# Performance work log

Measured on AMD Instinct MI355X. Metric: run time of the kernel, lower is better.

## Reference

```python
import jax, jax.numpy as jnp
import numpy as np

D_MODEL = 1024
N_HEADS = 16
D_K = D_MODEL // N_HEADS


def setup_inputs() -> dict:
    key = jax.random.key(0)
    ks = jax.random.split(key, 10)
    B, S = 4, 2048
    std = 1.0 / np.sqrt(D_MODEL)
    inp = {
        "x": jax.random.normal(ks[0], (B, S, D_MODEL), dtype=jnp.float32),
        "attention_mask": jnp.ones((B, S), dtype=jnp.int32),
        "W_q": jax.random.normal(ks[1], (D_MODEL, D_MODEL), dtype=jnp.float32) * std,
        "b_q": jnp.zeros((D_MODEL,), dtype=jnp.float32),
        "W_k": jax.random.normal(ks[2], (D_MODEL, D_MODEL), dtype=jnp.float32) * std,
        "b_k": jnp.zeros((D_MODEL,), dtype=jnp.float32),
        "W_v": jax.random.normal(ks[3], (D_MODEL, D_MODEL), dtype=jnp.float32) * std,
        "b_v": jnp.zeros((D_MODEL,), dtype=jnp.float32),
        "W_o": jax.random.normal(ks[4], (D_MODEL, D_MODEL), dtype=jnp.float32) * std,
        "b_o": jnp.zeros((D_MODEL,), dtype=jnp.float32),
    }
    return inp


def reference(x, attention_mask, W_q, b_q, W_k, b_k, W_v, b_v, W_o, b_o):
    B, S, _ = x.shape
    # projections -> [B, H, S, d_k]
    def proj(W, b):
        return (x @ W.T + b).reshape(B, S, N_HEADS, D_K).transpose(0, 2, 1, 3)
    q = proj(W_q, b_q)
    k = proj(W_k, b_k)
    v = proj(W_v, b_v)
    scores = jnp.einsum("bhqd,bhkd->bhqk", q, k) / jnp.sqrt(jnp.float32(D_K))
    mask = attention_mask[:, None, None, :] == 0  # [B,1,1,S]
    scores = jnp.where(mask, -jnp.inf, scores)
    probs = jax.nn.softmax(scores, axis=-1)  # dropout p=0 (eval)
    out = jnp.einsum("bhqk,bhkd->bhqd", probs, v)
    out = out.transpose(0, 2, 1, 3).reshape(B, S, D_MODEL)
    return out @ W_o.T + b_o
```

## Files before the change

kernel.cpp:

```cpp
#include <hip/hip_runtime.h>
#include <hip/hip_bf16.h>


#define SEQ   2048
#define DM    1024
#define NH    16
#define DK    64
#define MTOT  8192

typedef unsigned short u16;
typedef __attribute__((ext_vector_type(8))) short bf16x8;
typedef __attribute__((ext_vector_type(4))) float f32x4;

typedef union { unsigned u[4]; bf16x8 v; } FragU;

#define MFMA(a, b, c) __builtin_amdgcn_mfma_f32_16x16x32_bf16((a), (b), (c), 0, 0, 0)

#if __has_builtin(__builtin_amdgcn_exp2f)
#define EXP2(x) __builtin_amdgcn_exp2f(x)
#else
#define EXP2(x) __expf((x) * 0.69314718056f)
#endif

__device__ __forceinline__ u16 f2bf(float v) {
    unsigned int x = __float_as_uint(v);
    x += 0x7fffu + ((x >> 16) & 1u);
    return (u16)(x >> 16);
}
__device__ __forceinline__ float bf2f(u16 u) {
    return __uint_as_float(((unsigned int)u) << 16);
}
__device__ __forceinline__ unsigned pk2bf(float a, float b) {
    __hip_bfloat162 t = __float22bfloat162_rn(make_float2(a, b));
    unsigned r;
    __builtin_memcpy(&r, &t, 4);
    return r;
}

__device__ __forceinline__ void gl_lds16(const void* g, void* l) {
    __builtin_amdgcn_global_load_lds((__attribute__((address_space(1))) void*)g,
                                     (__attribute__((address_space(3))) void*)l,
                                     16, 0, 0);
}

__global__ __launch_bounds__(256) void split_f32(const float* __restrict__ src,
                                                 u16* __restrict__ dh,
                                                 u16* __restrict__ dl, int n4) {
    int i = blockIdx.x * 256 + threadIdx.x;
    if (i >= n4) return;
    float4 v = ((const float4*)src)[i];
    const float* f = (const float*)&v;
    ushort4 hh, ll;
    u16* hp = (u16*)&hh;
    u16* lp = (u16*)&ll;
#pragma unroll
    for (int j = 0; j < 4; ++j) {
        u16 h = f2bf(f[j]);
        hp[j] = h;
        lp[j] = f2bf(f[j] - bf2f(h));
    }
    ((ushort4*)dh)[i] = hh;
    ((ushort4*)dl)[i] = ll;
}

template <int MODE>
__global__ __launch_bounds__(256, 2) void gemm_split(
    const u16* __restrict__ Ah, const u16* __restrict__ Al,
    const u16* __restrict__ Bh, const u16* __restrict__ Bl,
    const float* __restrict__ bias,
    float* __restrict__ outF, u16* __restrict__ outH, u16* __restrict__ outL) {
    __shared__ u16 sm[4][128 * 64];

    const int tid = threadIdx.x;
    const int w = tid >> 6, lane = tid & 63;
    const int n0 = blockIdx.x * 128, m0 = blockIdx.y * 128;
    const int wr = w >> 1, wc = w & 1;
    const int rowoff = lane >> 3;
    const int cswz = ((lane & 7) ^ rowoff) << 3;

    const u16* src = (w == 0) ? Ah : (w == 1) ? Al : (w == 2) ? Bh : Bl;
    const int row0 = (w < 2) ? m0 : n0;
    const u16* sbase = src + (size_t)(row0 + rowoff) * 1024 + cswz;

    f32x4 acc[4][4];
#pragma unroll
    for (int a = 0; a < 4; ++a)
#pragma unroll
        for (int b = 0; b < 4; ++b) acc[a][b] = (f32x4)0.f;

    for (int k0 = 0; k0 < 1024; k0 += 64) {
#pragma unroll
        for (int i = 0; i < 16; ++i)
            gl_lds16(sbase + (size_t)(8 * i) * 1024 + k0, &sm[w][i * 512]);
        __syncthreads();
#pragma unroll
        for (int kk = 0; kk < 2; ++kk) {
            bf16x8 ah[4], al[4], bh[4], bl[4];
#pragma unroll
            for (int t = 0; t < 4; ++t) {
                const int Ra = wr * 64 + t * 16 + (lane & 15);
                const int oa = Ra * 128 + ((((kk << 2) + (lane >> 4)) ^ (Ra & 7)) << 4);
                ah[t] = *(const bf16x8*)((const char*)&sm[0][0] + oa);
                al[t] = *(const bf16x8*)((const char*)&sm[1][0] + oa);
                const int Rb = wc * 64 + t * 16 + (lane & 15);
                const int ob = Rb * 128 + ((((kk << 2) + (lane >> 4)) ^ (Rb & 7)) << 4);
                bh[t] = *(const bf16x8*)((const char*)&sm[2][0] + ob);
                bl[t] = *(const bf16x8*)((const char*)&sm[3][0] + ob);
            }
#pragma unroll
            for (int mt = 0; mt < 4; ++mt)
#pragma unroll
                for (int nt = 0; nt < 4; ++nt) {
                    acc[mt][nt] = MFMA(ah[mt], bh[nt], acc[mt][nt]);
                    acc[mt][nt] = MFMA(ah[mt], bl[nt], acc[mt][nt]);
                    acc[mt][nt] = MFMA(al[mt], bh[nt], acc[mt][nt]);
                }
        }
        __syncthreads();
    }

#pragma unroll
    for (int mt = 0; mt < 4; ++mt) {
#pragma unroll
        for (int nt = 0; nt < 4; ++nt) {
            const int n = n0 + wc * 64 + nt * 16 + (lane & 15);
            const float bv = bias[n];
#pragma unroll
            for (int j = 0; j < 4; ++j) {
                const int m = m0 + wr * 64 + mt * 16 + (lane >> 4) * 4 + j;
                const float v = acc[mt][nt][j] + bv;
                if (MODE == 0) {
                    outF[(size_t)m * 1024 + n] = v;
                } else {
                    const u16 h16 = f2bf(v);
                    const u16 l16 = f2bf(v - bf2f(h16));
                    const int b = m >> 11, s = m & 2047, hh = n >> 6, dk = n & 63;
                    size_t idx;
                    if (MODE == 1) idx = (((size_t)(b * 16 + hh)) * 2048 + s) * 64 + dk;
                    else           idx = (((size_t)(b * 16 + hh)) * 64 + dk) * 2048 + s;
                    outH[idx] = h16;
                    outL[idx] = l16;
                }
            }
        }
    }
}

__global__ __launch_bounds__(256, 2) void flash_mfma4(
    const u16* __restrict__ Qh, const u16* __restrict__ Ql,
    const u16* __restrict__ Kh, const u16* __restrict__ Kl,
    const u16* __restrict__ Vh, const u16* __restrict__ Vl,
    const int* __restrict__ amask,
    u16* __restrict__ Ch, u16* __restrict__ Cl) {
    __shared__ u16 sK[2][64 * 64];
    __shared__ u16 sV[2][64 * 64];
    __shared__ unsigned sMask[64];

    const int tid = threadIdx.x, w = tid >> 6, lane = tid & 63;
    const int i_flat = blockIdx.x + 16 * blockIdx.y;
    const int xcd = i_flat & 7, j_rem = i_flat >> 3;
    const int bh = xcd * 8 + (j_rem >> 4);
    const int qt = j_rem & 15;
    const int b = bh >> 4, h = bh & 15;
    const int q0 = qt * 128;
    const int hi = lane >> 4, l15 = lane & 15;
    const int rowoff = lane >> 3;
    const int cswz = ((lane & 7) ^ rowoff) << 3;
    const size_t kvbase = (size_t)bh * 2048;
    const float CE = 0.125f * 1.44269504089f;

    {
        const int* ap = amask + b * 2048 + tid * 8;
        int4 a0 = *(const int4*)ap;
        int4 a1 = *(const int4*)(ap + 4);
        unsigned byte = (unsigned)(a0.x != 0) | ((unsigned)(a0.y != 0) << 1) |
                        ((unsigned)(a0.z != 0) << 2) | ((unsigned)(a0.w != 0) << 3) |
                        ((unsigned)(a1.x != 0) << 4) | ((unsigned)(a1.y != 0) << 5) |
                        ((unsigned)(a1.z != 0) << 6) | ((unsigned)(a1.w != 0) << 7);
        ((unsigned char*)sMask)[tid] = (unsigned char)byte;
    }

    bf16x8 qfh[2][2], qfl[2][2];
#pragma unroll
    for (int st = 0; st < 2; ++st) {
        const size_t qrow = kvbase + q0 + w * 32 + st * 16 + l15;
        const int koff = hi * 8;
#pragma unroll
        for (int kk = 0; kk < 2; ++kk) {
            qfh[st][kk] = *(const bf16x8*)(Qh + qrow * 64 + kk * 32 + koff);
            qfl[st][kk] = *(const bf16x8*)(Ql + qrow * 64 + kk * 32 + koff);
        }
    }

    f32x4 o[2][4];
    float mi[2], li[2];
#pragma unroll
    for (int st = 0; st < 2; ++st) {
        mi[st] = -1e30f;
        li[st] = 0.f;
#pragma unroll
        for (int d = 0; d < 4; ++d) o[st][d] = (f32x4)0.f;
    }

    for (int kt = 0; kt < SEQ / 64; ++kt) {
        const int k0 = kt * 64;
        __syncthreads();
        {
            const u16* src = (w == 0) ? Kh : (w == 1) ? Kl : (w == 2) ? Vh : Vl;
            u16* dst = (w == 0) ? &sK[0][0] : (w == 1) ? &sK[1][0]
                     : (w == 2) ? &sV[0][0] : &sV[1][0];
            if (w < 2) {
                const u16* sb = src + (kvbase + k0 + rowoff) * 64 + cswz;
#pragma unroll
                for (int i = 0; i < 8; ++i)
                    gl_lds16(sb + (size_t)(8 * i) * 64, dst + i * 512);
            } else {
                const u16* sb = src + ((size_t)bh * 64 + rowoff) * 2048 + k0 + cswz;
#pragma unroll
                for (int i = 0; i < 8; ++i)
                    gl_lds16(sb + (size_t)(8 * i) * 2048, dst + i * 512);
            }
        }
        __syncthreads();

        f32x4 s[2][4];
#pragma unroll
        for (int st = 0; st < 2; ++st)
#pragma unroll
            for (int nt = 0; nt < 4; ++nt) s[st][nt] = (f32x4)0.f;
#pragma unroll
        for (int kk = 0; kk < 2; ++kk)
#pragma unroll
            for (int nt = 0; nt < 4; ++nt) {
                const int Rb = nt * 16 + l15;
                const int ob = Rb * 128 + ((((kk << 2) + hi) ^ (Rb & 7)) << 4);
                bf16x8 kbh = *(const bf16x8*)((const char*)&sK[0][0] + ob);
                bf16x8 kbl = *(const bf16x8*)((const char*)&sK[1][0] + ob);
                s[0][nt] = MFMA(kbh, qfh[0][kk], s[0][nt]);
                s[0][nt] = MFMA(kbh, qfl[0][kk], s[0][nt]);
                s[0][nt] = MFMA(kbl, qfh[0][kk], s[0][nt]);
                s[1][nt] = MFMA(kbh, qfh[1][kk], s[1][nt]);
                s[1][nt] = MFMA(kbh, qfl[1][kk], s[1][nt]);
                s[1][nt] = MFMA(kbl, qfh[1][kk], s[1][nt]);
            }

        const unsigned mlo = sMask[2 * kt], mhw = sMask[2 * kt + 1];
        if ((mlo & mhw) != 0xFFFFFFFFu) {
#pragma unroll
            for (int nt = 0; nt < 4; ++nt) {
                const unsigned mw = (nt & 2) ? mhw : mlo;
                const unsigned bits = mw >> (((nt & 1) << 4) + (hi << 2));
#pragma unroll
                for (int j = 0; j < 4; ++j)
                    if (!((bits >> j) & 1u)) {
                        s[0][nt][j] = -2e30f;
                        s[1][nt][j] = -2e30f;
                    }
            }
        }

        unsigned qph[2][4][2], qpl[2][4][2];
#pragma unroll
        for (int st = 0; st < 2; ++st) {
            float pm = s[st][0][0];
#pragma unroll
            for (int nt = 0; nt < 4; ++nt)
#pragma unroll
                for (int j = 0; j < 4; ++j) pm = fmaxf(pm, s[st][nt][j]);
            pm = fmaxf(pm, __shfl_xor(pm, 16));
            pm = fmaxf(pm, __shfl_xor(pm, 32));
            if (__any(pm > mi[st] + 64.f)) {
                const float mnew = fmaxf(mi[st], pm);
                const float sc = EXP2((mi[st] - mnew) * CE);
                li[st] *= sc;
#pragma unroll
                for (int d = 0; d < 4; ++d) o[st][d] *= sc;
                mi[st] = mnew;
            }
            const float nm = -mi[st] * CE;
            float p[4][4];
            float rs = 0.f;
#pragma unroll
            for (int nt = 0; nt < 4; ++nt)
#pragma unroll
                for (int j = 0; j < 4; ++j) {
                    const float e = EXP2(fmaf(s[st][nt][j], CE, nm));
                    p[nt][j] = e;
                    rs += e;
                }
            rs += __shfl_xor(rs, 16);
            rs += __shfl_xor(rs, 32);
            li[st] += rs;

#pragma unroll
            for (int nt = 0; nt < 4; ++nt)
#pragma unroll
                for (int c = 0; c < 2; ++c) {
                    const float v0 = p[nt][2 * c], v1 = p[nt][2 * c + 1];
                    const unsigned wh = pk2bf(v0, v1);
                    qph[st][nt][c] = wh;
                    const float r0 = v0 - __uint_as_float(wh << 16);
                    const float r1 = v1 - __uint_as_float(wh & 0xffff0000u);
                    qpl[st][nt][c] = pk2bf(r0, r1);
                }
        }

        const int src01 = l15 | ((lane & 16) << 1);
        const int src23 = src01 + 16;
#pragma unroll
        for (int kkv = 0; kkv < 2; ++kkv) {
            bf16x8 pbh[2], pbl[2];
#pragma unroll
            for (int st = 0; st < 2; ++st) {
                const unsigned ah0 = __shfl(qph[st][2 * kkv][0], src01);
                const unsigned ah1 = __shfl(qph[st][2 * kkv][1], src01);
                const unsigned ah2 = __shfl(qph[st][2 * kkv][0], src23);
                const unsigned ah3 = __shfl(qph[st][2 * kkv][1], src23);
                const unsigned bh0 = __shfl(qph[st][2 * kkv + 1][0], src01);
                const unsigned bh1 = __shfl(qph[st][2 * kkv + 1][1], src01);
                const unsigned bh2 = __shfl(qph[st][2 * kkv + 1][0], src23);
                const unsigned bh3 = __shfl(qph[st][2 * kkv + 1][1], src23);
                const unsigned al0 = __shfl(qpl[st][2 * kkv][0], src01);
                const unsigned al1 = __shfl(qpl[st][2 * kkv][1], src01);
                const unsigned al2 = __shfl(qpl[st][2 * kkv][0], src23);
                const unsigned al3 = __shfl(qpl[st][2 * kkv][1], src23);
                const unsigned bl0 = __shfl(qpl[st][2 * kkv + 1][0], src01);
                const unsigned bl1 = __shfl(qpl[st][2 * kkv + 1][1], src01);
                const unsigned bl2 = __shfl(qpl[st][2 * kkv + 1][0], src23);
                const unsigned bl3 = __shfl(qpl[st][2 * kkv + 1][1], src23);
                const bool up = (hi >= 2);
                FragU uh, ul;
                uh.u[0] = up ? bh0 : ah0;
                uh.u[1] = up ? bh1 : ah1;
                uh.u[2] = up ? bh2 : ah2;
                uh.u[3] = up ? bh3 : ah3;
                ul.u[0] = up ? bl0 : al0;
                ul.u[1] = up ? bl1 : al1;
                ul.u[2] = up ? bl2 : al2;
                ul.u[3] = up ? bl3 : al3;
                pbh[st] = uh.v;
                pbl[st] = ul.v;
            }
#pragma unroll
            for (int ntd = 0; ntd < 4; ++ntd) {
                const int Rv = ntd * 16 + l15;
                const int ov = Rv * 128 + ((((kkv << 2) + hi) ^ (Rv & 7)) << 4);
                bf16x8 vbh = *(const bf16x8*)((const char*)&sV[0][0] + ov);
                bf16x8 vbl = *(const bf16x8*)((const char*)&sV[1][0] + ov);
                o[0][ntd] = MFMA(vbh, pbh[0], o[0][ntd]);
                o[0][ntd] = MFMA(vbh, pbl[0], o[0][ntd]);
                o[0][ntd] = MFMA(vbl, pbh[0], o[0][ntd]);
                o[1][ntd] = MFMA(vbh, pbh[1], o[1][ntd]);
                o[1][ntd] = MFMA(vbh, pbl[1], o[1][ntd]);
                o[1][ntd] = MFMA(vbl, pbh[1], o[1][ntd]);
            }
        }
    }

#pragma unroll
    for (int st = 0; st < 2; ++st) {
        const float inv = 1.f / li[st];
        const int srow = q0 + w * 32 + st * 16 + l15;
        const size_t obase = ((size_t)b * 2048 + srow) * 1024 + h * 64;
#pragma unroll
        for (int ntd = 0; ntd < 4; ++ntd) {
            const float v0 = o[st][ntd][0] * inv, v1 = o[st][ntd][1] * inv;
            const float v2 = o[st][ntd][2] * inv, v3 = o[st][ntd][3] * inv;
            const unsigned wh0 = pk2bf(v0, v1), wh1 = pk2bf(v2, v3);
            const float r0 = v0 - __uint_as_float(wh0 << 16);
            const float r1 = v1 - __uint_as_float(wh0 & 0xffff0000u);
            const float r2 = v2 - __uint_as_float(wh1 << 16);
            const float r3 = v3 - __uint_as_float(wh1 & 0xffff0000u);
            const unsigned wl0 = pk2bf(r0, r1), wl1 = pk2bf(r2, r3);
            const size_t idx = obase + ntd * 16 + hi * 4;
            uint2 sh, sl;
            sh.x = wh0; sh.y = wh1;
            sl.x = wl0; sl.y = wl1;
            *(uint2*)&Ch[idx] = sh;
            *(uint2*)&Cl[idx] = sl;
        }
    }
}

extern "C" void kernel_launch(void* const* d_in, const int* in_sizes, int n_in,
                              void* d_out, int out_size, void* d_ws, size_t ws_size,
                              hipStream_t stream) {
    const float* x  = (const float*)d_in[0];
    const int* am   = (const int*)d_in[1];
    const float* Wq = (const float*)d_in[2];
    const float* bq = (const float*)d_in[3];
    const float* Wk = (const float*)d_in[4];
    const float* bk = (const float*)d_in[5];
    const float* Wv = (const float*)d_in[6];
    const float* bv = (const float*)d_in[7];
    const float* Wo = (const float*)d_in[8];
    const float* bo = (const float*)d_in[9];
    float* out = (float*)d_out;

    const size_t MB = 1u << 20;
    char* ws = (char*)d_ws;
    u16* Xh  = (u16*)(ws + 0 * MB);
    u16* Xl  = (u16*)(ws + 16 * MB);
    u16* qh  = (u16*)(ws + 32 * MB);
    u16* ql  = (u16*)(ws + 48 * MB);
    u16* kh  = (u16*)(ws + 64 * MB);
    u16* kl  = (u16*)(ws + 80 * MB);
    u16* vh  = (u16*)(ws + 96 * MB);
    u16* vl  = (u16*)(ws + 112 * MB);
    u16* Wqh = (u16*)(ws + 128 * MB);
    u16* Wql = (u16*)(ws + 130 * MB);
    u16* Wkh = (u16*)(ws + 132 * MB);
    u16* Wkl = (u16*)(ws + 134 * MB);
    u16* Wvh = (u16*)(ws + 136 * MB);
    u16* Wvl = (u16*)(ws + 138 * MB);
    u16* Woh = (u16*)(ws + 140 * MB);
    u16* Wol = (u16*)(ws + 142 * MB);

    split_f32<<<(MTOT * DM / 4 + 255) / 256, 256, 0, stream>>>(x, Xh, Xl, MTOT * DM / 4);
    split_f32<<<(DM * DM / 4 + 255) / 256, 256, 0, stream>>>(Wq, Wqh, Wql, DM * DM / 4);
    split_f32<<<(DM * DM / 4 + 255) / 256, 256, 0, stream>>>(Wk, Wkh, Wkl, DM * DM / 4);
    split_f32<<<(DM * DM / 4 + 255) / 256, 256, 0, stream>>>(Wv, Wvh, Wvl, DM * DM / 4);
    split_f32<<<(DM * DM / 4 + 255) / 256, 256, 0, stream>>>(Wo, Woh, Wol, DM * DM / 4);

    dim3 ggrid(DM / 128, MTOT / 128);
    gemm_split<1><<<ggrid, 256, 0, stream>>>(Xh, Xl, Wqh, Wql, bq, nullptr, qh, ql);
    gemm_split<1><<<ggrid, 256, 0, stream>>>(Xh, Xl, Wkh, Wkl, bk, nullptr, kh, kl);
    gemm_split<2><<<ggrid, 256, 0, stream>>>(Xh, Xl, Wvh, Wvl, bv, nullptr, vh, vl);

    flash_mfma4<<<dim3(SEQ / 128, 4 * NH), 256, 0, stream>>>(qh, ql, kh, kl, vh, vl, am, Xh, Xl);

    gemm_split<0><<<ggrid, 256, 0, stream>>>(Xh, Xl, Woh, Wol, bo, out, nullptr, nullptr);
}
```

Measured before the change: 549.3 us.

## Double-buffer K/V tiles in LDS to overlap loads with attention compute

The flash attention kernel now keeps two LDS buffers each for K and V. At the start of each iteration it issues the async global-to-LDS copies for the next tile, then computes on the current one. This drops one of the two barriers per iteration and hides load latency behind the MFMA work. In exchange, LDS use doubles to about 64KB per block, which may put the two-blocks-per-CU occupancy target under pressure.

Result: slower. 601.9 us (+9.6%).

```diff
diff --git a/kernel.cpp b/kernel.cpp
--- a/kernel.cpp
+++ b/kernel.cpp
@@ -146,14 +146,14 @@
     }
 }
 
-__global__ __launch_bounds__(256, 2) void flash_mfma4(
+__global__ __launch_bounds__(256, 2) void flash_mfma5(
     const u16* __restrict__ Qh, const u16* __restrict__ Ql,
     const u16* __restrict__ Kh, const u16* __restrict__ Kl,
     const u16* __restrict__ Vh, const u16* __restrict__ Vl,
     const int* __restrict__ amask,
     u16* __restrict__ Ch, u16* __restrict__ Cl) {
-    __shared__ u16 sK[2][64 * 64];
-    __shared__ u16 sV[2][64 * 64];
+    __shared__ u16 sK[2][2][64 * 64];
+    __shared__ u16 sV[2][2][64 * 64];
     __shared__ unsigned sMask[64];
 
     const int tid = threadIdx.x, w = tid >> 6, lane = tid & 63;
@@ -192,6 +192,29 @@
         }
     }
 
+    const u16* ssrc = (w == 0) ? Kh : (w == 1) ? Kl : (w == 2) ? Vh : Vl;
+    u16* sdst[2];
+    sdst[0] = (w == 0) ? &sK[0][0][0] : (w == 1) ? &sK[0][1][0]
+            : (w == 2) ? &sV[0][0][0] : &sV[0][1][0];
+    sdst[1] = (w == 0) ? &sK[1][0][0] : (w == 1) ? &sK[1][1][0]
+            : (w == 2) ? &sV[1][0][0] : &sV[1][1][0];
+
+    auto stage = [&](int buf, int ktile) {
+        const int k0 = ktile * 64;
+        u16* dst = sdst[buf];
+        if (w < 2) {
+            const u16* sb = ssrc + (kvbase + k0 + rowoff) * 64 + cswz;
+#pragma unroll
+            for (int i = 0; i < 8; ++i)
+                gl_lds16(sb + (size_t)(8 * i) * 64, dst + i * 512);
+        } else {
+            const u16* sb = ssrc + ((size_t)bh * 64 + rowoff) * 2048 + k0 + cswz;
+#pragma unroll
+            for (int i = 0; i < 8; ++i)
+                gl_lds16(sb + (size_t)(8 * i) * 2048, dst + i * 512);
+        }
+    };
+
     f32x4 o[2][4];
     float mi[2], li[2];
 #pragma unroll
@@ -202,26 +225,17 @@
         for (int d = 0; d < 4; ++d) o[st][d] = (f32x4)0.f;
     }
 
+    stage(0, 0);
+    __syncthreads();
+
     for (int kt = 0; kt < SEQ / 64; ++kt) {
-        const int k0 = kt * 64;
-        __syncthreads();
-        {
-            const u16* src = (w == 0) ? Kh : (w == 1) ? Kl : (w == 2) ? Vh : Vl;
-            u16* dst = (w == 0) ? &sK[0][0] : (w == 1) ? &sK[1][0]
-                     : (w == 2) ? &sV[0][0] : &sV[1][0];
-            if (w < 2) {
-                const u16* sb = src + (kvbase + k0 + rowoff) * 64 + cswz;
-#pragma unroll
-                for (int i = 0; i < 8; ++i)
-                    gl_lds16(sb + (size_t)(8 * i) * 64, dst + i * 512);
-            } else {
-                const u16* sb = src + ((size_t)bh * 64 + rowoff) * 2048 + k0 + cswz;
-#pragma unroll
-                for (int i = 0; i < 8; ++i)
-                    gl_lds16(sb + (size_t)(8 * i) * 2048, dst + i * 512);
-            }
-        }
-        __syncthreads();
+        const int cur = kt & 1;
+        if (kt + 1 < SEQ / 64) stage(cur ^ 1, kt + 1);
+
+        const u16* sKh = &sK[cur][0][0];
+        const u16* sKl = &sK[cur][1][0];
+        const u16* sVh = &sV[cur][0][0];
+        const u16* sVl = &sV[cur][1][0];
 
         f32x4 s[2][4];
 #pragma unroll
@@ -234,8 +248,8 @@
             for (int nt = 0; nt < 4; ++nt) {
                 const int Rb = nt * 16 + l15;
                 const int ob = Rb * 128 + ((((kk << 2) + hi) ^ (Rb & 7)) << 4);
-                bf16x8 kbh = *(const bf16x8*)((const char*)&sK[0][0] + ob);
-                bf16x8 kbl = *(const bf16x8*)((const char*)&sK[1][0] + ob);
+                bf16x8 kbh = *(const bf16x8*)((const char*)sKh + ob);
+                bf16x8 kbl = *(const bf16x8*)((const char*)sKl + ob);
                 s[0][nt] = MFMA(kbh, qfh[0][kk], s[0][nt]);
                 s[0][nt] = MFMA(kbh, qfl[0][kk], s[0][nt]);
                 s[0][nt] = MFMA(kbl, qfh[0][kk], s[0][nt]);
@@ -345,8 +359,8 @@
             for (int ntd = 0; ntd < 4; ++ntd) {
                 const int Rv = ntd * 16 + l15;
                 const int ov = Rv * 128 + ((((kkv << 2) + hi) ^ (Rv & 7)) << 4);
-                bf16x8 vbh = *(const bf16x8*)((const char*)&sV[0][0] + ov);
-                bf16x8 vbl = *(const bf16x8*)((const char*)&sV[1][0] + ov);
+                bf16x8 vbh = *(const bf16x8*)((const char*)sVh + ov);
+                bf16x8 vbl = *(const bf16x8*)((const char*)sVl + ov);
                 o[0][ntd] = MFMA(vbh, pbh[0], o[0][ntd]);
                 o[0][ntd] = MFMA(vbh, pbl[0], o[0][ntd]);
                 o[0][ntd] = MFMA(vbl, pbh[0], o[0][ntd]);
@@ -355,6 +369,8 @@
                 o[1][ntd] = MFMA(vbl, pbh[1], o[1][ntd]);
             }
         }
+
+        __syncthreads();
     }
 
 #pragma unroll
@@ -427,7 +443,7 @@
     gemm_split<1><<<ggrid, 256, 0, stream>>>(Xh, Xl, Wkh, Wkl, bk, nullptr, kh, kl);
     gemm_split<2><<<ggrid, 256, 0, stream>>>(Xh, Xl, Wvh, Wvl, bv, nullptr, vh, vl);
 
-    flash_mfma4<<<dim3(SEQ / 128, 4 * NH), 256, 0, stream>>>(qh, ql, kh, kl, vh, vl, am, Xh, Xl);
+    flash_mfma5<<<dim3(SEQ / 128, 4 * NH), 256, 0, stream>>>(qh, ql, kh, kl, vh, vl, am, Xh, Xl);
 
     gemm_split<0><<<ggrid, 256, 0, stream>>>(Xh, Xl, Woh, Wol, bo, out, nullptr, nullptr);
 }
```
